# Kernel optimization log

Measured on AMD Instinct MI355X. Metric: run time of the kernel, lower is better.

## Reference

```python
import jax, jax.numpy as jnp
import numpy as np

N_NODES = 50000
N_EDGES = 800000
IN_CH = 64
HID = 128
OUT_CH = 1
NUM_LAYERS = 3
NUM_TIMESTEPS = 3
EDGE_DIM = 25
NUM_GRAPHS = 1024
NEG = 0.01  # leaky_relu negative slope (torch default & GATConv arg)


def leaky(v):
    return jnp.where(v >= 0, v, NEG * v)


def seg_softmax(a, idx, n):
    # PyG softmax: exp(a - max_per_segment) / (sum_per_segment + 1e-16)
    m = jax.ops.segment_max(a, idx, num_segments=n)
    m = jnp.where(jnp.isfinite(m), m, 0.0)  # guard empty segments
    e = jnp.exp(a - m[idx])
    s = jax.ops.segment_sum(e, idx, num_segments=n)
    return e / (s[idx] + 1e-16)


def gru(inp, h, Wih, Whh, bih, bhh):
    gi = inp @ Wih.T + bih
    gh = h @ Whh.T + bhh
    ir, iz, inn = jnp.split(gi, 3, axis=-1)
    hr, hz, hn = jnp.split(gh, 3, axis=-1)
    r = jax.nn.sigmoid(ir + hr)
    z = jax.nn.sigmoid(iz + hz)
    n = jnp.tanh(inn + r * hn)
    return (1.0 - z) * n + z * h


def setup_inputs() -> dict:
    key = jax.random.key(0)
    ks = iter(jax.random.split(key, 40))

    def nrm(shape, s=0.05):
        return jax.random.normal(next(ks), shape, dtype=jnp.float32) * s

    L = NUM_LAYERS - 1
    H3 = 3 * HID
    inp = dict(
        x=jax.random.normal(next(ks), (N_NODES, IN_CH), dtype=jnp.float32),
        edge_index=jax.random.randint(next(ks), (2, N_EDGES), 0, N_NODES),
        batch=jnp.sort(jax.random.randint(next(ks), (N_NODES,), 0, NUM_GRAPHS)),
        W1=nrm((HID, IN_CH)), b1=jnp.zeros((HID,), jnp.float32),
        Wg1=nrm((HID, HID + EDGE_DIM)), att_l=nrm((HID,)), att_r=nrm((HID,)),
        Wg2=nrm((HID, HID)), bg=jnp.zeros((HID,), jnp.float32),
        Wih0=nrm((H3, HID)), Whh0=nrm((H3, HID)),
        bih0=jnp.zeros((H3,), jnp.float32), bhh0=jnp.zeros((H3,), jnp.float32),
        Wa=nrm((L, HID, HID)), att_src_a=nrm((L, HID)), att_dst_a=nrm((L, HID)),
        ba=jnp.zeros((L, HID), jnp.float32),
        Wih_a=nrm((L, H3, HID)), Whh_a=nrm((L, H3, HID)),
        bih_a=jnp.zeros((L, H3), jnp.float32), bhh_a=jnp.zeros((L, H3), jnp.float32),
        Wm=nrm((HID, HID)), att_src_m=nrm((HID,)), att_dst_m=nrm((HID,)),
        bm=jnp.zeros((HID,), jnp.float32),
        Wih_m=nrm((H3, HID)), Whh_m=nrm((H3, HID)),
        bih_m=jnp.zeros((H3,), jnp.float32), bhh_m=jnp.zeros((H3,), jnp.float32),
        W2=nrm((OUT_CH, HID)), b2=jnp.zeros((OUT_CH,), jnp.float32),
    )
    return inp


def reference(x, edge_index, batch, W1, b1, Wg1, att_l, att_r, Wg2, bg,
              Wih0, Whh0, bih0, bhh0, Wa, att_src_a, att_dst_a, ba,
              Wih_a, Whh_a, bih_a, bhh_a, Wm, att_src_m, att_dst_m, bm,
              Wih_m, Whh_m, bih_m, bhh_m, W2, b2):
    N = x.shape[0]
    E = edge_index.shape[1]
    src, dst = edge_index[0], edge_index[1]  # j -> i, aggregate at i=dst
    edge_attr = jnp.ones((E, EDGE_DIM), dtype=x.dtype)  # built inside original forward

    x = leaky(x @ W1.T + b1)

    # GATEConv: edge-feature-aware attention, sum aggregation
    xe = leaky(jnp.concatenate([x[src], edge_attr], axis=-1) @ Wg1.T)  # [E, H]
    a = seg_softmax(leaky(xe @ att_l + (x @ att_r)[dst]), dst, N)
    msg = (x[src] @ Wg2.T) * a[:, None]
    h = jax.nn.elu(jax.ops.segment_sum(msg, dst, num_segments=N) + bg)
    x = jax.nn.relu(gru(h, x, Wih0, Whh0, bih0, bhh0))

    # (num_layers - 1) GATConv + GRU atom updates
    for l in range(NUM_LAYERS - 1):
        xt = x @ Wa[l].T
        a = seg_softmax(leaky((xt @ att_src_a[l])[src] + (xt @ att_dst_a[l])[dst]), dst, N)
        h = jax.nn.elu(jax.ops.segment_sum(xt[src] * a[:, None], dst, num_segments=N) + ba[l])
        x = jax.nn.relu(gru(h, x, Wih_a[l], Whh_a[l], bih_a[l], bhh_a[l]))

    # attentive readout: bipartite GATConv node->molecule over num_timesteps
    out = jax.nn.relu(jax.ops.segment_sum(x, batch, num_segments=NUM_GRAPHS))
    xt = x @ Wm.T                 # shared lin for src (fixed across timesteps)
    a_src = xt @ att_src_m        # [N]
    for _ in range(NUM_TIMESTEPS):
        ot = out @ Wm.T           # shared lin for dst
        a = seg_softmax(leaky(a_src + (ot @ att_dst_m)[batch]), batch, NUM_GRAPHS)
        h = jax.nn.elu(jax.ops.segment_sum(xt * a[:, None], batch, num_segments=NUM_GRAPHS) + bm)
        out = jax.nn.relu(gru(h, out, Wih_m, Whh_m, bih_m, bhh_m))

    return out @ W2.T + b2
```

## Files before the change

### kernel.cpp

```cpp
#include <hip/hip_runtime.h>
#include <math.h>

#define NN 50000
#define NE 800000
#define NG 1024
#define HID 128

typedef __attribute__((ext_vector_type(8))) short short8;
typedef __attribute__((ext_vector_type(4))) unsigned short ushort4v;
typedef __attribute__((ext_vector_type(4))) float f32x4;

__device__ __forceinline__ float leakyf(float v){ return v >= 0.f ? v : 0.01f*v; }
__device__ __forceinline__ float frcp(float x){ return __builtin_amdgcn_rcpf(x); }
__device__ __forceinline__ float fsigm(float v){ return frcp(1.f + __expf(-v)); }
__device__ __forceinline__ float ftanh(float v){ return 1.f - 2.f*frcp(1.f + __expf(2.f*v)); }
__device__ __forceinline__ float eluf(float v){ return v > 0.f ? v : __expf(v) - 1.f; }
__device__ __forceinline__ unsigned short bf16rne(float f){
  union { float f; unsigned u; } v; v.f = f;
  return (unsigned short)((v.u + 0x7FFFu + ((v.u >> 16) & 1u)) >> 16);
}
__device__ __forceinline__ float bf2f(unsigned short h){
  union { unsigned u; float f; } v; v.u = ((unsigned)h) << 16; return v.f;
}
__device__ __forceinline__ short8 cvt8(const float* a){
  short8 r;
#pragma unroll
  for (int j=0;j<8;j++) r[j] = (short)bf16rne(a[j]);
  return r;
}

__global__ __launch_bounds__(256)
void pack_all(const float* W1, const float* Wg1, const float* Wg2, const float* Wa,
              const float* Wm, const float* Wih0, const float* Whh0,
              const float* Wih_a, const float* Whh_a,
              unsigned short* __restrict__ dst)
{
  int m = (int)blockIdx.y;
  int t = (int)blockIdx.x*4 + ((int)threadIdx.x>>6);
  int l = (int)threadIdx.x & 63;
  const float* src; int stride=128, M=128, K=128; size_t doff;
  switch(m){
    case 0:  src=W1;    stride=64;  K=64;  doff=0;      break;
    case 1:  src=Wg1;   stride=153;        doff=8192;   break;
    case 2:  src=Wg2;                      doff=24576;  break;
    case 3:  src=Wa;                       doff=40960;  break;
    case 4:  src=Wa+16384;                 doff=57344;  break;
    case 5:  src=Wm;                       doff=73728;  break;
    case 6:  src=Wih0;  M=384;             doff=90112;  break;
    case 7:  src=Whh0;  M=384;             doff=139264; break;
    case 8:  src=Wih_a; M=384;             doff=188416; break;
    case 9:  src=Whh_a; M=384;             doff=237568; break;
    case 10: src=Wih_a+49152; M=384;       doff=286720; break;
    default: src=Whh_a+49152; M=384;       doff=335872; break;
  }
  int tk = K/32;
  if (t >= (M/16)*tk) return;
  int ct = t / tk, kc = t % tk;
  int row = ct*16 + (l&15);
  int col = kc*32 + ((l>>4)<<3);
  unsigned short o[8];
#pragma unroll
  for (int j=0;j<8;j++) o[j] = bf16rne(src[(size_t)row*stride + col + j]);
  ushort4v* d = (ushort4v*)(dst + doff + (((size_t)t*64 + l)<<3));
  ushort4v d0; d0.x=o[0]; d0.y=o[1]; d0.z=o[2]; d0.w=o[3];
  ushort4v d1; d1.x=o[4]; d1.y=o[5]; d1.z=o[6]; d1.w=o[7];
  d[0]=d0; d[1]=d1;
}

__global__ void pack_t(const float* __restrict__ Wi, const float* __restrict__ Wh,
                       unsigned short* __restrict__ Wit, unsigned short* __restrict__ Wht)
{
  int k = (int)blockIdx.x;
  int cg = (int)threadIdx.x + (int)blockIdx.y*128;
  Wit[(size_t)k*384 + cg] = bf16rne(Wi[(size_t)cg*128 + k]);
  Wht[(size_t)k*384 + cg] = bf16rne(Wh[(size_t)cg*128 + k]);
}

__global__ __launch_bounds__(256)
void gemm_f32(const float* __restrict__ A, const unsigned short* __restrict__ Wp,
              const float* __restrict__ bias, float* __restrict__ Cf,
              unsigned short* __restrict__ Cb, int rows, int act)
{
  constexpr int K = 64, KC = 2;
  const int tid=(int)threadIdx.x, w=tid>>6, l=tid&63;
  const int fr=l&15, fq=l>>4;
  const int rt=w>>1, ch=w&1;
  const int bn = (int)blockIdx.x*32;
  const int ar = bn + rt*16 + fr;
  f32x4 acc[4];
#pragma unroll
  for (int j=0;j<4;j++) acc[j] = (f32x4){0.f,0.f,0.f,0.f};
#pragma unroll
  for (int kc=0;kc<KC;kc++){
    float a8[8];
    if (ar < rows){
      *(float4*)&a8[0] = *(const float4*)(A + (size_t)ar*K + kc*32 + fq*8);
      *(float4*)&a8[4] = *(const float4*)(A + (size_t)ar*K + kc*32 + fq*8 + 4);
    } else {
#pragma unroll
      for (int j=0;j<8;j++) a8[j]=0.f;
    }
    short8 fa = cvt8(a8);
#pragma unroll
    for (int j=0;j<4;j++){
      const short8 bfr = *(const short8*)(Wp + ((((size_t)(ch*4+j)*KC + kc)*64 + l)<<3));
      acc[j] = __builtin_amdgcn_mfma_f32_16x16x32_bf16(fa, bfr, acc[j], 0, 0, 0);
    }
  }
#pragma unroll
  for (int j=0;j<4;j++){
    int c = ch*64 + j*16 + fr;
    float bv = bias ? bias[c] : 0.f;
#pragma unroll
    for (int r4=0;r4<4;r4++){
      float o = acc[j][r4] + bv;
      if (act) o = leakyf(o);
      int r = bn + rt*16 + fq*4 + r4;
      if (r < rows){
        Cf[(size_t)r*HID + c] = o;
        Cb[(size_t)r*HID + c] = bf16rne(o);
      }
    }
  }
}

__global__ __launch_bounds__(256)
void gemm_b16(const unsigned short* __restrict__ Ab, const unsigned short* __restrict__ Wp,
              const float* __restrict__ bias, unsigned short* __restrict__ Cb,
              const float* __restrict__ v1, const float* __restrict__ v2,
              float* __restrict__ s1, float* __restrict__ s2, int rows, int act)
{
  __shared__ float sd1[2][32];
  __shared__ float sd2[2][32];
  constexpr int KC = 4;
  const int tid=(int)threadIdx.x, w=tid>>6, l=tid&63;
  const int fr=l&15, fq=l>>4;
  const int rt=w>>1, ch=w&1;
  const int bn = (int)blockIdx.x*32;
  const int ar = bn + rt*16 + fr;
  f32x4 acc[4];
#pragma unroll
  for (int j=0;j<4;j++) acc[j] = (f32x4){0.f,0.f,0.f,0.f};
#pragma unroll
  for (int kc=0;kc<KC;kc++){
    short8 fa;
    if (ar < rows) fa = *(const short8*)(Ab + (size_t)ar*HID + kc*32 + fq*8);
    else { short8 z = {0,0,0,0,0,0,0,0}; fa = z; }
#pragma unroll
    for (int j=0;j<4;j++){
      const short8 bfr = *(const short8*)(Wp + ((((size_t)(ch*4+j)*KC + kc)*64 + l)<<3));
      acc[j] = __builtin_amdgcn_mfma_f32_16x16x32_bf16(fa, bfr, acc[j], 0, 0, 0);
    }
  }
  float dp1[4]={0.f,0.f,0.f,0.f}, dp2[4]={0.f,0.f,0.f,0.f};
#pragma unroll
  for (int j=0;j<4;j++){
    int c = ch*64 + j*16 + fr;
    float bv = bias ? bias[c] : 0.f;
    float w1 = v1 ? v1[c] : 0.f;
    float w2 = v2 ? v2[c] : 0.f;
#pragma unroll
    for (int r4=0;r4<4;r4++){
      float o = acc[j][r4] + bv;
      if (act) o = leakyf(o);
      dp1[r4] += o*w1; dp2[r4] += o*w2;
      int r = bn + rt*16 + fq*4 + r4;
      if (r < rows && Cb) Cb[(size_t)r*HID + c] = bf16rne(o);
    }
  }
  if (v1){
#pragma unroll
    for (int r4=0;r4<4;r4++){
#pragma unroll
      for (int m=1;m<16;m<<=1){ dp1[r4] += __shfl_xor(dp1[r4], m); dp2[r4] += __shfl_xor(dp2[r4], m); }
    }
    if (fr==0){
#pragma unroll
      for (int r4=0;r4<4;r4++){
        sd1[ch][rt*16 + fq*4 + r4] = dp1[r4];
        sd2[ch][rt*16 + fq*4 + r4] = dp2[r4];
      }
    }
    __syncthreads();
    if (tid < 32){
      int r = bn + tid;
      if (r < rows) s1[r] = sd1[0][tid] + sd1[1][tid];
    } else if (v2 && tid < 64){
      int r = bn + tid - 32;
      if (r < rows) s2[r] = sd2[0][tid-32] + sd2[1][tid-32];
    }
  }
}

__global__ __launch_bounds__(256)
void gemm_gate(const unsigned short* __restrict__ Ab,
               const unsigned short* __restrict__ W1p, const unsigned short* __restrict__ W2p,
               const float* __restrict__ cg, const float* __restrict__ attl,
               const float* __restrict__ attr,
               unsigned short* __restrict__ Cb,
               float* __restrict__ s1, float* __restrict__ s2, int rows)
{
  __shared__ float sd1[2][32];
  constexpr int KC = 4;
  const int tid=(int)threadIdx.x, w=tid>>6, l=tid&63;
  const int fr=l&15, fq=l>>4;
  const int rt=w>>1, ch=w&1;
  const int bn = (int)blockIdx.x*32;
  const int ar = bn + rt*16 + fr;
  f32x4 acc1[4], acc2[4];
#pragma unroll
  for (int j=0;j<4;j++){ acc1[j]=(f32x4){0,0,0,0}; acc2[j]=(f32x4){0,0,0,0}; }
  float pa = 0.f;
#pragma unroll
  for (int kc=0;kc<KC;kc++){
    short8 fa;
    if (ar < rows) fa = *(const short8*)(Ab + (size_t)ar*HID + kc*32 + fq*8);
    else { short8 z = {0,0,0,0,0,0,0,0}; fa = z; }
    if (ch==0){
      float4 t0 = *(const float4*)(attr + kc*32 + fq*8);
      float4 t1 = *(const float4*)(attr + kc*32 + fq*8 + 4);
      pa += bf2f((unsigned short)fa[0])*t0.x + bf2f((unsigned short)fa[1])*t0.y
          + bf2f((unsigned short)fa[2])*t0.z + bf2f((unsigned short)fa[3])*t0.w
          + bf2f((unsigned short)fa[4])*t1.x + bf2f((unsigned short)fa[5])*t1.y
          + bf2f((unsigned short)fa[6])*t1.z + bf2f((unsigned short)fa[7])*t1.w;
    }
#pragma unroll
    for (int j=0;j<4;j++){
      size_t wo = ((((size_t)(ch*4+j)*KC + kc)*64 + l)<<3);
      acc1[j] = __builtin_amdgcn_mfma_f32_16x16x32_bf16(fa, *(const short8*)(W1p + wo), acc1[j], 0, 0, 0);
      acc2[j] = __builtin_amdgcn_mfma_f32_16x16x32_bf16(fa, *(const short8*)(W2p + wo), acc2[j], 0, 0, 0);
    }
  }
  float dp1[4]={0.f,0.f,0.f,0.f};
#pragma unroll
  for (int j=0;j<4;j++){
    int c = ch*64 + j*16 + fr;
    float bv = cg[c];
    float w1 = attl[c];
#pragma unroll
    for (int r4=0;r4<4;r4++){
      float o1 = leakyf(acc1[j][r4] + bv);
      dp1[r4] += o1*w1;
      int r = bn + rt*16 + fq*4 + r4;
      if (r < rows) Cb[(size_t)r*HID + c] = bf16rne(acc2[j][r4]);
    }
  }
#pragma unroll
  for (int r4=0;r4<4;r4++){
#pragma unroll
    for (int m=1;m<16;m<<=1) dp1[r4] += __shfl_xor(dp1[r4], m);
  }
  if (fr==0){
#pragma unroll
    for (int r4=0;r4<4;r4++) sd1[ch][rt*16 + fq*4 + r4] = dp1[r4];
  }
  __syncthreads();
  if (tid < 32){
    int r = bn + tid;
    if (r < rows) s1[r] = sd1[0][tid] + sd1[1][tid];
  }
  if (ch==0){
    pa += __shfl_xor(pa, 16); pa += __shfl_xor(pa, 32);
    if (fq==0){
      int r = bn + rt*16 + fr;
      if (r < rows) s2[r] = pa;
    }
  }
}

#define GRU_TPB 4
__global__ __launch_bounds__(512, 2)
void fused_gru(const unsigned short* __restrict__ Ahb, const unsigned short* __restrict__ Axb,
               const float* __restrict__ Axf,
               const unsigned short* __restrict__ Wi, const unsigned short* __restrict__ Wh,
               const float* __restrict__ bih, const float* __restrict__ bhh,
               float* __restrict__ outf, unsigned short* __restrict__ outb, int tiles)
{
  const int tid=(int)threadIdx.x, w=tid>>6, l=tid&63;
  const int fr=l&15, fq=l>>4;
  short8 wi_r[3][4], wh_r[3][4];
#pragma unroll
  for (int g=0;g<3;g++)
#pragma unroll
    for (int kc=0;kc<4;kc++){
      size_t o = ((((size_t)(g*8 + w)*4 + kc)*64 + l)<<3);
      wi_r[g][kc] = *(const short8*)(Wi + o);
      wh_r[g][kc] = *(const short8*)(Wh + o);
    }
  const int c0 = w*16 + fr;
  float bi0=bih[c0], bi1=bih[c0+128], bi2=bih[c0+256];
  float bh0=bhh[c0], bh1=bhh[c0+128], bh2=bhh[c0+256];

  int rt = (int)blockIdx.x*GRU_TPB;
  int rt_end = min(rt + GRU_TPB, tiles);
  if (rt >= tiles) return;
  short8 fa[4], fx[4];
  {
    const int arow = rt*16 + fr;
#pragma unroll
    for (int kc=0;kc<4;kc++){
      fa[kc] = *(const short8*)(Ahb + (size_t)arow*HID + kc*32 + fq*8);
      fx[kc] = *(const short8*)(Axb + (size_t)arow*HID + kc*32 + fq*8);
    }
  }
  for (; rt < rt_end; rt++){
    short8 nfa[4], nfx[4];
    if (rt+1 < rt_end){
      const int arow = (rt+1)*16 + fr;
#pragma unroll
      for (int kc=0;kc<4;kc++){
        nfa[kc] = *(const short8*)(Ahb + (size_t)arow*HID + kc*32 + fq*8);
        nfx[kc] = *(const short8*)(Axb + (size_t)arow*HID + kc*32 + fq*8);
      }
    }
    float hv[4];
#pragma unroll
    for (int r4=0;r4<4;r4++) hv[r4] = Axf[(size_t)(rt*16 + fq*4 + r4)*HID + c0];

    f32x4 ai0={0,0,0,0}, ai1={0,0,0,0}, ai2={0,0,0,0};
    f32x4 ah0={0,0,0,0}, ah1={0,0,0,0}, ah2={0,0,0,0};
#pragma unroll
    for (int kc=0;kc<4;kc++){
      ai0 = __builtin_amdgcn_mfma_f32_16x16x32_bf16(fa[kc], wi_r[0][kc], ai0, 0, 0, 0);
      ai1 = __builtin_amdgcn_mfma_f32_16x16x32_bf16(fa[kc], wi_r[1][kc], ai1, 0, 0, 0);
      ai2 = __builtin_amdgcn_mfma_f32_16x16x32_bf16(fa[kc], wi_r[2][kc], ai2, 0, 0, 0);
      ah0 = __builtin_amdgcn_mfma_f32_16x16x32_bf16(fx[kc], wh_r[0][kc], ah0, 0, 0, 0);
      ah1 = __builtin_amdgcn_mfma_f32_16x16x32_bf16(fx[kc], wh_r[1][kc], ah1, 0, 0, 0);
      ah2 = __builtin_amdgcn_mfma_f32_16x16x32_bf16(fx[kc], wh_r[2][kc], ah2, 0, 0, 0);
    }
#pragma unroll
    for (int r4=0;r4<4;r4++){
      int row = rt*16 + fq*4 + r4;
      float rr = fsigm(ai0[r4] + bi0 + ah0[r4] + bh0);
      float zz = fsigm(ai1[r4] + bi1 + ah1[r4] + bh1);
      float nn = ftanh(ai2[r4] + bi2 + rr*(ah2[r4] + bh2));
      float o = fmaxf((1.f - zz)*nn + zz*hv[r4], 0.f);
      outf[(size_t)row*HID + c0] = o;
      outb[(size_t)row*HID + c0] = bf16rne(o);
    }
#pragma unroll
    for (int kc=0;kc<4;kc++){ fa[kc]=nfa[kc]; fx[kc]=nfx[kc]; }
  }
}

__global__ void colvec(const float* __restrict__ W, const float* __restrict__ v,
                       float* __restrict__ out)
{
  int k = (int)threadIdx.x;
  float s = 0.f;
  for (int j=0;j<HID;j++) s += W[j*HID+k]*v[j];
  out[k] = s;
}

__global__ void prep_cg(const float* __restrict__ Wg1, float* __restrict__ cg){
  int j = (int)threadIdx.x;
  float s = 0.f;
  for (int k=128;k<153;k++) s += Wg1[j*153+k];
  cg[j] = s;
}

__global__ void count_kernel(const int* __restrict__ idx, int* __restrict__ cnt, int n){
  int i = (int)(blockIdx.x*blockDim.x + threadIdx.x);
  if (i < n) atomicAdd(&cnt[idx[i]], 1);
}

__global__ __launch_bounds__(1024)
void scan_blocks(const int* __restrict__ cnt, int* __restrict__ off,
                 int* __restrict__ tot, int n)
{
  __shared__ int buf[1024];
  int i = (int)(blockIdx.x*1024 + threadIdx.x);
  int v = (i<n)? cnt[i] : 0;
  buf[threadIdx.x] = v;
  __syncthreads();
  for (int s=1;s<1024;s<<=1){
    int t = ((int)threadIdx.x >= s) ? buf[threadIdx.x - s] : 0;
    __syncthreads();
    buf[threadIdx.x] += t;
    __syncthreads();
  }
  if (i<n) off[i] = buf[threadIdx.x] - v;
  if (threadIdx.x==1023) tot[blockIdx.x] = buf[1023];
}

__global__ void scan_tot(int* __restrict__ tot, int* __restrict__ off_end, int nb){
  int lane = (int)threadIdx.x;
  int orig = (lane<nb)? tot[lane] : 0;
  int v = orig;
  for (int s=1;s<64;s<<=1){ int t = __shfl_up(v, s); if (lane>=s) v += t; }
  int total = __shfl(v, 63);
  if (lane<nb) tot[lane] = v - orig;
  if (lane==0) *off_end = total;
}

__global__ void scan_add(int* __restrict__ off, int* __restrict__ off_mut,
                         const int* __restrict__ tot, int n){
  int i = (int)(blockIdx.x*blockDim.x + threadIdx.x);
  if (i<n){
    int v = off[i] + tot[i>>10];
    off[i] = v;
    off_mut[i] = v;
  }
}

__global__ void fill_kernel(const int* __restrict__ src, const int* __restrict__ dst,
                            int* __restrict__ off_mut, int* __restrict__ ssrc, int n){
  int e = (int)(blockIdx.x*blockDim.x + threadIdx.x);
  if (e < n){
    int p = atomicAdd(&off_mut[dst[e]], 1);
    ssrc[p] = src[e];
  }
}

__global__ void graph_bounds(const int* __restrict__ batch, int* __restrict__ goff){
  int g = (int)(blockIdx.x*blockDim.x + threadIdx.x);
  if (g > NG) return;
  int lo=0, hi=NN;
  while (lo<hi){ int mid=(lo+hi)>>1; if (batch[mid] < g) lo=mid+1; else hi=mid; }
  goff[g] = lo;
}

__global__ __launch_bounds__(256)
void agg_edges(const int* __restrict__ off, const int* __restrict__ ssrc,
               const float* __restrict__ ls, const float* __restrict__ ld,
               const unsigned short* __restrict__ Mrows, const float* __restrict__ bias,
               unsigned short* __restrict__ outb, int n)
{
  __shared__ float wbuf[4][64];
  __shared__ int   sbuf[4][64];
  const int ws = (int)(threadIdx.x >> 6);
  int node = (int)((blockIdx.x * blockDim.x + threadIdx.x) >> 6);
  int lane = (int)(threadIdx.x & 63);
  if (node >= n) return;
  int e0 = off[node], e1 = off[node+1];
  float ldv = ld[node];
  const int g4 = lane >> 4, cl = lane & 15;
  float denom = 0.f;
  float acc[8] = {0.f,0.f,0.f,0.f,0.f,0.f,0.f,0.f};
  for (int j0=e0; j0<e1; j0+=64){
    int cnt = min(64, e1-j0);
    float wv = 0.f; int sc = 0;
    if (lane < cnt){
      sc = ssrc[j0+lane];
      wv = __expf(leakyf(ls[sc]+ldv));
    }
    denom += wv;
    wbuf[ws][lane] = wv;
    sbuf[ws][lane] = sc;
#pragma unroll 2
    for (int k4=0;k4<cnt;k4+=4){
      float wk = wbuf[ws][k4+g4];
      int  sck = sbuf[ws][k4+g4];
      uint4 mm = *(const uint4*)(Mrows + (size_t)sck*HID + cl*8);
      acc[0] += wk*bf2f((unsigned short)(mm.x&0xffff));
      acc[1] += wk*bf2f((unsigned short)(mm.x>>16));
      acc[2] += wk*bf2f((unsigned short)(mm.y&0xffff));
      acc[3] += wk*bf2f((unsigned short)(mm.y>>16));
      acc[4] += wk*bf2f((unsigned short)(mm.z&0xffff));
      acc[5] += wk*bf2f((unsigned short)(mm.z>>16));
      acc[6] += wk*bf2f((unsigned short)(mm.w&0xffff));
      acc[7] += wk*bf2f((unsigned short)(mm.w>>16));
    }
  }
#pragma unroll
  for (int j=0;j<8;j++){ acc[j] += __shfl_xor(acc[j], 16); acc[j] += __shfl_xor(acc[j], 32); }
  for (int o=32;o;o>>=1) denom += __shfl_xor(denom, o);
  if (g4==0){
    float inv = frcp(denom + 1e-16f);
    float4 b0 = *(const float4*)(bias + cl*8);
    float4 b1 = *(const float4*)(bias + cl*8 + 4);
    float o0=eluf(acc[0]*inv+b0.x), o1=eluf(acc[1]*inv+b0.y);
    float o2=eluf(acc[2]*inv+b0.z), o3=eluf(acc[3]*inv+b0.w);
    float o4=eluf(acc[4]*inv+b1.x), o5=eluf(acc[5]*inv+b1.y);
    float o6=eluf(acc[6]*inv+b1.z), o7=eluf(acc[7]*inv+b1.w);
    uint4 u;
    u.x = (unsigned)bf16rne(o0) | ((unsigned)bf16rne(o1)<<16);
    u.y = (unsigned)bf16rne(o2) | ((unsigned)bf16rne(o3)<<16);
    u.z = (unsigned)bf16rne(o4) | ((unsigned)bf16rne(o5)<<16);
    u.w = (unsigned)bf16rne(o6) | ((unsigned)bf16rne(o7)<<16);
    *(uint4*)(outb + (size_t)node*HID + cl*8) = u;
  }
}

__global__ __launch_bounds__(128)
void readout_all(const int* __restrict__ goff, const float* __restrict__ X,
                 const float* __restrict__ asrc, const unsigned short* __restrict__ Xt,
                 const float* __restrict__ vmd, const float* __restrict__ bm_,
                 const unsigned short* __restrict__ Wit, const unsigned short* __restrict__ Wht,
                 const float* __restrict__ bih, const float* __restrict__ bhh,
                 const float* __restrict__ W2, const float* __restrict__ b2,
                 float* __restrict__ dout)
{
  __shared__ float sh_h[128];
  __shared__ float sh_o[128];
  __shared__ float sred[2];
  const int g = (int)blockIdx.x, c = (int)threadIdx.x;
  const int n0 = goff[g], n1 = goff[g+1];
  float a0=0.f,a1=0.f,a2=0.f,a3=0.f;
  int n = n0;
  for (; n+4<=n1; n+=4){
    a0 += X[(size_t)(n+0)*HID+c]; a1 += X[(size_t)(n+1)*HID+c];
    a2 += X[(size_t)(n+2)*HID+c]; a3 += X[(size_t)(n+3)*HID+c];
  }
  for (; n<n1; ++n) a0 += X[(size_t)n*HID+c];
  float ov = fmaxf((a0+a1)+(a2+a3), 0.f);
  const float bi0=bih[c], bi1=bih[c+128], bi2=bih[c+256];
  const float bh0=bhh[c], bh1=bhh[c+128], bh2=bhh[c+256];
  const float vm = vmd[c], bmc = bm_[c];
  for (int t=0;t<3;t++){
    float p = ov*vm;
    for (int o=32;o;o>>=1) p += __shfl_down(p, o);
    if ((c&63)==0) sred[c>>6] = p;
    __syncthreads();
    float ad = sred[0] + sred[1];
    float denom = 0.f, acc = 0.f;
    for (int nn=n0; nn<n1; ++nn){
      float wv = __expf(leakyf(asrc[nn] + ad));
      denom += wv;
      acc += wv * bf2f(Xt[(size_t)nn*HID + c]);
    }
    float h = eluf(acc*frcp(denom + 1e-16f) + bmc);
    __syncthreads();
    sh_h[c] = h; sh_o[c] = ov;
    __syncthreads();
    float gi0=0.f,gi1=0.f,gi2=0.f,gh0=0.f,gh1=0.f,gh2=0.f;
    for (int k=0;k<128;k++){
      float hk = sh_h[k], ok = sh_o[k];
      const unsigned short* wi = Wit + (size_t)k*384;
      const unsigned short* wh = Wht + (size_t)k*384;
      gi0 += bf2f(wi[c])*hk;  gi1 += bf2f(wi[c+128])*hk;  gi2 += bf2f(wi[c+256])*hk;
      gh0 += bf2f(wh[c])*ok;  gh1 += bf2f(wh[c+128])*ok;  gh2 += bf2f(wh[c+256])*ok;
    }
    float rr = fsigm(gi0+bi0+gh0+bh0);
    float zz = fsigm(gi1+bi1+gh1+bh1);
    float nv = ftanh(gi2+bi2 + rr*(gh2+bh2));
    ov = fmaxf((1.f-zz)*nv + zz*ov, 0.f);
  }
  float p = ov*W2[c];
  for (int o=32;o;o>>=1) p += __shfl_down(p, o);
  __syncthreads();
  if ((c&63)==0) sred[c>>6] = p;
  __syncthreads();
  if (c==0) dout[g] = sred[0] + sred[1] + b2[0];
}

extern "C" void kernel_launch(void* const* d_in, const int* in_sizes, int n_in,
                              void* d_out, int out_size, void* d_ws, size_t ws_size,
                              hipStream_t stream)
{
  const float* x_in  = (const float*)d_in[0];
  const int*   ei    = (const int*)d_in[1];
  const int*   batch = (const int*)d_in[2];
  const float* W1    = (const float*)d_in[3];
  const float* b1    = (const float*)d_in[4];
  const float* Wg1   = (const float*)d_in[5];
  const float* att_l = (const float*)d_in[6];
  const float* att_r = (const float*)d_in[7];
  const float* Wg2   = (const float*)d_in[8];
  const float* bg    = (const float*)d_in[9];
  const float* Wih0  = (const float*)d_in[10];
  const float* Whh0  = (const float*)d_in[11];
  const float* bih0  = (const float*)d_in[12];
  const float* bhh0  = (const float*)d_in[13];
  const float* Wa    = (const float*)d_in[14];
  const float* att_src_a = (const float*)d_in[15];
  const float* att_dst_a = (const float*)d_in[16];
  const float* ba    = (const float*)d_in[17];
  const float* Wih_a = (const float*)d_in[18];
  const float* Whh_a = (const float*)d_in[19];
  const float* bih_a = (const float*)d_in[20];
  const float* bhh_a = (const float*)d_in[21];
  const float* Wm    = (const float*)d_in[22];
  const float* att_src_m = (const float*)d_in[23];
  const float* att_dst_m = (const float*)d_in[24];
  const float* bm    = (const float*)d_in[25];
  const float* Wih_m = (const float*)d_in[26];
  const float* Whh_m = (const float*)d_in[27];
  const float* bih_m = (const float*)d_in[28];
  const float* bhh_m = (const float*)d_in[29];
  const float* W2    = (const float*)d_in[30];
  const float* b2    = (const float*)d_in[31];
  (void)in_sizes; (void)n_in; (void)out_size; (void)ws_size;

  char* wsb = (char*)d_ws;
  size_t off = 0;
  auto alloc = [&](size_t bytes)->void* {
    void* p = wsb + off;
    off += (bytes + 255) & ~(size_t)255;
    return p;
  };
  float* f_x   = (float*)alloc((size_t)NN*HID*4);
  float* f_y   = (float*)alloc((size_t)NN*HID*4);
  unsigned short* f_xb = (unsigned short*)alloc((size_t)NN*HID*2);
  unsigned short* f_yb = (unsigned short*)alloc((size_t)NN*HID*2);
  unsigned short* f_h  = (unsigned short*)alloc((size_t)NN*HID*2);
  unsigned short* f_t  = (unsigned short*)alloc((size_t)NN*HID*2);
  float* f_s1  = (float*)alloc((size_t)NN*4);
  float* f_s2  = (float*)alloc((size_t)NN*4);
  float* w_cg  = (float*)alloc((size_t)HID*4);
  float* w_vmd = (float*)alloc((size_t)HID*4);
  unsigned short* w_pack = (unsigned short*)alloc((size_t)385024*2);
  unsigned short* w_wit  = (unsigned short*)alloc((size_t)49152*2);
  unsigned short* w_wht  = (unsigned short*)alloc((size_t)49152*2);
  int* i_cnt   = (int*)alloc((size_t)NN*4);
  int* i_off   = (int*)alloc((size_t)(NN+1)*4);
  int* i_offm  = (int*)alloc((size_t)NN*4);
  int* i_src   = (int*)alloc((size_t)NE*4);
  int* i_tot   = (int*)alloc((size_t)64*4);
  int* i_goff  = (int*)alloc((size_t)(NG+1)*4);

  const unsigned short* pk_W1   = w_pack + 0;
  const unsigned short* pk_g1   = w_pack + 8192;
  const unsigned short* pk_g2   = w_pack + 24576;
  const unsigned short* pk_wa0  = w_pack + 40960;
  const unsigned short* pk_wa1  = w_pack + 57344;
  const unsigned short* pk_wm   = w_pack + 73728;
  const unsigned short* pk_wih0 = w_pack + 90112;
  const unsigned short* pk_whh0 = w_pack + 139264;
  const unsigned short* pk_wiha0= w_pack + 188416;
  const unsigned short* pk_whha0= w_pack + 237568;
  const unsigned short* pk_wiha1= w_pack + 286720;
  const unsigned short* pk_whha1= w_pack + 335872;

  const int* e_src = ei;
  const int* e_dst = ei + NE;

  hipMemsetAsync(i_cnt, 0, (size_t)NN*4, stream);

  const int NB = (NN + 1023)/1024;
  count_kernel<<<(NE+255)/256,256,0,stream>>>(e_dst, i_cnt, NE);
  scan_blocks<<<NB,1024,0,stream>>>(i_cnt, i_off, i_tot, NN);
  scan_tot<<<1,64,0,stream>>>(i_tot, i_off+NN, NB);
  scan_add<<<(NN+255)/256,256,0,stream>>>(i_off, i_offm, i_tot, NN);
  fill_kernel<<<(NE+255)/256,256,0,stream>>>(e_src, e_dst, i_offm, i_src, NE);
  graph_bounds<<<(NG+1+255)/256,256,0,stream>>>(batch, i_goff);
  prep_cg<<<1,128,0,stream>>>(Wg1, w_cg);
  colvec<<<1,128,0,stream>>>(Wm, att_dst_m, w_vmd);
  pack_all<<<dim3(24,12),256,0,stream>>>(W1, Wg1, Wg2, Wa, Wm, Wih0, Whh0,
                                         Wih_a, Whh_a, w_pack);
  pack_t<<<dim3(128,3),128,0,stream>>>(Wih_m, Whh_m, w_wit, w_wht);

  const int GB = (NN+31)/32;
  const int NT = NN/16;
  const int FB = (NT+GRU_TPB-1)/GRU_TPB;

  gemm_f32<<<GB,256,0,stream>>>(x_in, pk_W1, b1, f_x, f_xb, NN, 1);

  float* curf = f_x;  unsigned short* curb = f_xb;
  float* nxtf = f_y;  unsigned short* nxtb = f_yb;

  gemm_gate<<<GB,256,0,stream>>>(curb, pk_g1, pk_g2, w_cg, att_l, att_r,
                                 f_t, f_s1, f_s2, NN);
  agg_edges<<<(NN+3)/4,256,0,stream>>>(i_off, i_src, f_s1, f_s2, f_t, bg, f_h, NN);
  fused_gru<<<FB,512,0,stream>>>(f_h, curb, curf, pk_wih0, pk_whh0, bih0, bhh0,
                                 nxtf, nxtb, NT);
  { float* t=curf; curf=nxtf; nxtf=t; unsigned short* tb=curb; curb=nxtb; nxtb=tb; }

  for (int l=0;l<2;l++){
    gemm_b16<<<GB,256,0,stream>>>(curb, l ? pk_wa1 : pk_wa0, nullptr, f_t,
                                  att_src_a + l*HID, att_dst_a + l*HID,
                                  f_s1, f_s2, NN, 0);
    agg_edges<<<(NN+3)/4,256,0,stream>>>(i_off, i_src, f_s1, f_s2, f_t, ba + l*HID, f_h, NN);
    fused_gru<<<FB,512,0,stream>>>(f_h, curb, curf,
                                   l ? pk_wiha1 : pk_wiha0, l ? pk_whha1 : pk_whha0,
                                   bih_a + l*384, bhh_a + l*384, nxtf, nxtb, NT);
    { float* t=curf; curf=nxtf; nxtf=t; unsigned short* tb=curb; curb=nxtb; nxtb=tb; }
  }

  gemm_b16<<<GB,256,0,stream>>>(curb, pk_wm, nullptr, f_t,
                                att_src_m, nullptr, f_s1, nullptr, NN, 0);
  readout_all<<<NG,128,0,stream>>>(i_goff, curf, f_s1, f_t, w_vmd, bm,
                                   w_wit, w_wht, bih_m, bhh_m, W2, b2,
                                   (float*)d_out);
}
```

Before: 618.6 us.

## Split readout work across four thread groups and prefetch GRU hidden state

The readout kernel now runs 512 threads per graph instead of 128. Node sums, the attention aggregation and the GRU matvec over k are split four ways and reduced through shared memory, which raises parallelism for the serial per-graph loops. The node GRU kernel also prefetches the fp32 hidden-state values for the next tile along with the bf16 fragments. The cost is more shared-memory traffic and extra barriers, plus more registers spent on prefetching.

```diff
diff --git a/kernel.cpp b/kernel.cpp
--- a/kernel.cpp
+++ b/kernel.cpp
@@ -295,6 +295,7 @@
   int rt_end = min(rt + GRU_TPB, tiles);
   if (rt >= tiles) return;
   short8 fa[4], fx[4];
+  float hv[4];
   {
     const int arow = rt*16 + fr;
 #pragma unroll
@@ -302,9 +303,12 @@
       fa[kc] = *(const short8*)(Ahb + (size_t)arow*HID + kc*32 + fq*8);
       fx[kc] = *(const short8*)(Axb + (size_t)arow*HID + kc*32 + fq*8);
     }
+#pragma unroll
+    for (int r4=0;r4<4;r4++) hv[r4] = Axf[(size_t)(rt*16 + fq*4 + r4)*HID + c0];
   }
   for (; rt < rt_end; rt++){
     short8 nfa[4], nfx[4];
+    float nhv[4];
     if (rt+1 < rt_end){
       const int arow = (rt+1)*16 + fr;
 #pragma unroll
@@ -312,11 +316,9 @@
         nfa[kc] = *(const short8*)(Ahb + (size_t)arow*HID + kc*32 + fq*8);
         nfx[kc] = *(const short8*)(Axb + (size_t)arow*HID + kc*32 + fq*8);
       }
-    }
-    float hv[4];
-#pragma unroll
-    for (int r4=0;r4<4;r4++) hv[r4] = Axf[(size_t)(rt*16 + fq*4 + r4)*HID + c0];
-
+#pragma unroll
+      for (int r4=0;r4<4;r4++) nhv[r4] = Axf[(size_t)((rt+1)*16 + fq*4 + r4)*HID + c0];
+    }
     f32x4 ai0={0,0,0,0}, ai1={0,0,0,0}, ai2={0,0,0,0};
     f32x4 ah0={0,0,0,0}, ah1={0,0,0,0}, ah2={0,0,0,0};
 #pragma unroll
@@ -340,6 +342,8 @@
     }
 #pragma unroll
     for (int kc=0;kc<4;kc++){ fa[kc]=nfa[kc]; fx[kc]=nfx[kc]; }
+#pragma unroll
+    for (int r4=0;r4<4;r4++) hv[r4]=nhv[r4];
   }
 }
 
@@ -482,7 +486,7 @@
   }
 }
 
-__global__ __launch_bounds__(128)
+__global__ __launch_bounds__(512)
 void readout_all(const int* __restrict__ goff, const float* __restrict__ X,
                  const float* __restrict__ asrc, const unsigned short* __restrict__ Xt,
                  const float* __restrict__ vmd, const float* __restrict__ bm_,
@@ -491,57 +495,86 @@
                  const float* __restrict__ W2, const float* __restrict__ b2,
                  float* __restrict__ dout)
 {
+  __shared__ float sh_o[128];
   __shared__ float sh_h[128];
-  __shared__ float sh_o[128];
-  __shared__ float sred[2];
-  const int g = (int)blockIdx.x, c = (int)threadIdx.x;
+  __shared__ float sp[4][128];
+  __shared__ float sg[6][4][128];
+  __shared__ float sden[4];
+  __shared__ float sred[4];
+  const int g = (int)blockIdx.x;
+  const int tid = (int)threadIdx.x;
+  const int c = tid & 127, s = tid >> 7;
   const int n0 = goff[g], n1 = goff[g+1];
-  float a0=0.f,a1=0.f,a2=0.f,a3=0.f;
-  int n = n0;
-  for (; n+4<=n1; n+=4){
-    a0 += X[(size_t)(n+0)*HID+c]; a1 += X[(size_t)(n+1)*HID+c];
-    a2 += X[(size_t)(n+2)*HID+c]; a3 += X[(size_t)(n+3)*HID+c];
-  }
-  for (; n<n1; ++n) a0 += X[(size_t)n*HID+c];
-  float ov = fmaxf((a0+a1)+(a2+a3), 0.f);
+
+  float a = 0.f;
+  for (int n = n0 + s; n < n1; n += 4) a += X[(size_t)n*HID + c];
+  sp[s][c] = a;
+  __syncthreads();
+  if (s == 0)
+    sh_o[c] = fmaxf(sp[0][c]+sp[1][c]+sp[2][c]+sp[3][c], 0.f);
+  __syncthreads();
+
   const float bi0=bih[c], bi1=bih[c+128], bi2=bih[c+256];
   const float bh0=bhh[c], bh1=bhh[c+128], bh2=bhh[c+256];
-  const float vm = vmd[c], bmc = bm_[c];
+  const float bmc = bm_[c];
+
   for (int t=0;t<3;t++){
-    float p = ov*vm;
-    for (int o=32;o;o>>=1) p += __shfl_down(p, o);
-    if ((c&63)==0) sred[c>>6] = p;
+    if (s == 0){
+      float p = sh_o[c]*vmd[c];
+      for (int o=32;o;o>>=1) p += __shfl_down(p, o);
+      if ((c&63)==0) sred[c>>6] = p;
+    }
     __syncthreads();
     float ad = sred[0] + sred[1];
-    float denom = 0.f, acc = 0.f;
-    for (int nn=n0; nn<n1; ++nn){
+    float den = 0.f, acc = 0.f;
+    for (int nn = n0 + s; nn < n1; nn += 4){
       float wv = __expf(leakyf(asrc[nn] + ad));
-      denom += wv;
+      den += wv;
       acc += wv * bf2f(Xt[(size_t)nn*HID + c]);
     }
-    float h = eluf(acc*frcp(denom + 1e-16f) + bmc);
+    sp[s][c] = acc;
+    if (c == 0) sden[s] = den;
     __syncthreads();
-    sh_h[c] = h; sh_o[c] = ov;
+    if (s == 0){
+      float dsum = sden[0]+sden[1]+sden[2]+sden[3];
+      float asum = sp[0][c]+sp[1][c]+sp[2][c]+sp[3][c];
+      sh_h[c] = eluf(asum*frcp(dsum + 1e-16f) + bmc);
+    }
     __syncthreads();
     float gi0=0.f,gi1=0.f,gi2=0.f,gh0=0.f,gh1=0.f,gh2=0.f;
-    for (int k=0;k<128;k++){
+    const int k0 = s*32;
+#pragma unroll 4
+    for (int k=k0;k<k0+32;k++){
       float hk = sh_h[k], ok = sh_o[k];
       const unsigned short* wi = Wit + (size_t)k*384;
       const unsigned short* wh = Wht + (size_t)k*384;
-      gi0 += bf2f(wi[c])*hk;  gi1 += bf2f(wi[c+128])*hk;  gi2 += bf2f(wi[c+256])*hk;
-      gh0 += bf2f(wh[c])*ok;  gh1 += bf2f(wh[c+128])*ok;  gh2 += bf2f(wh[c+256])*ok;
-    }
-    float rr = fsigm(gi0+bi0+gh0+bh0);
-    float zz = fsigm(gi1+bi1+gh1+bh1);
-    float nv = ftanh(gi2+bi2 + rr*(gh2+bh2));
-    ov = fmaxf((1.f-zz)*nv + zz*ov, 0.f);
-  }
-  float p = ov*W2[c];
-  for (int o=32;o;o>>=1) p += __shfl_down(p, o);
+      gi0 += bf2f(wi[c])*hk; gi1 += bf2f(wi[c+128])*hk; gi2 += bf2f(wi[c+256])*hk;
+      gh0 += bf2f(wh[c])*ok; gh1 += bf2f(wh[c+128])*ok; gh2 += bf2f(wh[c+256])*ok;
+    }
+    sg[0][s][c]=gi0; sg[1][s][c]=gi1; sg[2][s][c]=gi2;
+    sg[3][s][c]=gh0; sg[4][s][c]=gh1; sg[5][s][c]=gh2;
+    __syncthreads();
+    if (s == 0){
+      float G0=sg[0][0][c]+sg[0][1][c]+sg[0][2][c]+sg[0][3][c];
+      float G1=sg[1][0][c]+sg[1][1][c]+sg[1][2][c]+sg[1][3][c];
+      float G2=sg[2][0][c]+sg[2][1][c]+sg[2][2][c]+sg[2][3][c];
+      float H0=sg[3][0][c]+sg[3][1][c]+sg[3][2][c]+sg[3][3][c];
+      float H1=sg[4][0][c]+sg[4][1][c]+sg[4][2][c]+sg[4][3][c];
+      float H2=sg[5][0][c]+sg[5][1][c]+sg[5][2][c]+sg[5][3][c];
+      float rr = fsigm(G0+bi0+H0+bh0);
+      float zz = fsigm(G1+bi1+H1+bh1);
+      float nv = ftanh(G2+bi2 + rr*(H2+bh2));
+      sh_o[c] = fmaxf((1.f-zz)*nv + zz*sh_o[c], 0.f);
+    }
+    __syncthreads();
+  }
+  if (s == 0){
+    float p = sh_o[c]*W2[c];
+    for (int o=32;o;o>>=1) p += __shfl_down(p, o);
+    if ((c&63)==0) sred[(c>>6)+2] = p;
+  }
   __syncthreads();
-  if ((c&63)==0) sred[c>>6] = p;
-  __syncthreads();
-  if (c==0) dout[g] = sred[0] + sred[1] + b2[0];
+  if (tid==0) dout[g] = sred[2] + sred[3] + b2[0];
 }
 
 extern "C" void kernel_launch(void* const* d_in, const int* in_sizes, int n_in,
@@ -669,7 +702,7 @@
 
   gemm_b16<<<GB,256,0,stream>>>(curb, pk_wm, nullptr, f_t,
                                 att_src_m, nullptr, f_s1, nullptr, NN, 0);
-  readout_all<<<NG,128,0,stream>>>(i_goff, curf, f_s1, f_t, w_vmd, bm,
+  readout_all<<<NG,512,0,stream>>>(i_goff, curf, f_s1, f_t, w_vmd, bm,
                                    w_wit, w_wht, bih_m, bhh_m, W2, b2,
                                    (float*)d_out);
 }
```

Result: faster. 596.0 us (-3.7%).
